# Kernel optimization log

Measured on AMD Instinct MI355X. Metric: run time of the kernel, lower is better.

Reference implementation:

```python
import jax, jax.numpy as jnp
import numpy as np

N_IN = 41024
N_OUT = 256


def setup_inputs() -> dict:
    key = jax.random.key(0)
    k1, k2, k3, k4 = jax.random.split(key, 4)
    B, K = 16384, 32
    ft_ics = jax.random.randint(k1, (B, K), 0, N_IN, dtype=jnp.int32)
    ft_vals = jax.random.uniform(k2, (B, K), dtype=jnp.float32)
    s = N_IN ** (-0.5)
    weight = jax.random.uniform(k3, (N_IN, N_OUT), dtype=jnp.float32) * (2 * s) - s
    bias = jax.random.uniform(k4, (N_OUT,), dtype=jnp.float32) * (2 * s) - s
    return {"ft_ics": ft_ics, "ft_vals": ft_vals, "weight": weight, "bias": bias}


def reference(ft_ics, ft_vals, weight, bias):
    # Sparse embedding-bag: out[b] = bias + sum_k weight[ft_ics[b,k]] * ft_vals[b,k]
    # ft_ics == -1 marks padding (the CUDA kernel breaks on -1); mask those.
    valid = ft_ics >= 0                                  # [B, K]
    safe_idx = jnp.where(valid, ft_ics, 0)               # in-range for gather
    vals = jnp.where(valid, ft_vals, 0.0)                # [B, K]
    gathered = weight[safe_idx]                          # [B, K, N_OUT]
    out = jnp.einsum("bk,bkd->bd", vals, gathered) + bias
    return out
```

## Files before the change

kernel.cpp:

```cpp
#include <hip/hip_runtime.h>


constexpr int K = 32;

__global__ __launch_bounds__(256) void FeatureTransformer_45896020525219_kernel(
    const int* __restrict__ ics,
    const float* __restrict__ vals,
    const float4* __restrict__ w4,
    const float4* __restrict__ bias4,
    float4* __restrict__ out4,
    int B)
{
    const int lane   = threadIdx.x & 63;
    const int wave   = threadIdx.x >> 6;
    const int slice  = blockIdx.x & 7;
    const int rowblk = blockIdx.x >> 3;

    const int r  = lane >> 3;
    const int c4 = lane & 7;
    const int b  = rowblk * 32 + wave * 8 + r;
    if (b >= B) return;

    const int colbase = slice * 8 + c4;

    const int4   idx4 = ((const int4*)  (ics  + b * K))[c4];
    const float4 v4   = ((const float4*)(vals + b * K))[c4];

    float4 acc = bias4[colbase];

    #pragma unroll
    for (int k = 0; k < K; ++k) {
        const int src = (lane & 56) | (k >> 2);
        const int   sel = k & 3;
        const int   jc  = sel == 0 ? idx4.x : sel == 1 ? idx4.y
                        : sel == 2 ? idx4.z : idx4.w;
        const float vc  = sel == 0 ? v4.x   : sel == 1 ? v4.y
                        : sel == 2 ? v4.z   : v4.w;
        const int   jj = __shfl(jc, src);
        const float vs = __shfl(vc, src);

        const float    v = (jj >= 0) ? vs : 0.0f;
        const unsigned j = (jj >= 0) ? (unsigned)jj : 0u;

        const float4 w = w4[(size_t)j * 64 + colbase];
        acc.x = fmaf(v, w.x, acc.x);
        acc.y = fmaf(v, w.y, acc.y);
        acc.z = fmaf(v, w.z, acc.z);
        acc.w = fmaf(v, w.w, acc.w);
    }

    out4[(size_t)b * 64 + colbase] = acc;
}

extern "C" void kernel_launch(void* const* d_in, const int* in_sizes, int n_in,
                              void* d_out, int out_size, void* d_ws, size_t ws_size,
                              hipStream_t stream) {
    const int*    ics   = (const int*)d_in[0];
    const float*  vals  = (const float*)d_in[1];
    const float4* w4    = (const float4*)d_in[2];
    const float4* bias4 = (const float4*)d_in[3];
    float4*       out4  = (float4*)d_out;

    const int B = in_sizes[0] / K;
    const int blocks = ((B + 31) / 32) * 8;

    hipLaunchKernelGGL(FeatureTransformer_45896020525219_kernel,
                       dim3(blocks), dim3(256), 0, stream,
                       ics, vals, w4, bias4, out4, B);
}
```

Measured before the change: 126.2 us.

## Process four rows per thread and load indices directly instead of shuffling

Each thread now accumulates four output rows spaced 32 apart, so every block covers 128 rows and the grid shrinks by a factor of four. The cross-lane shuffles that handed out indices and values are gone. Each thread reads the index and value vectors for its own rows directly (redundant loads, broadcast within each 8-lane group), which exposes four independent weight gathers per step for more memory-level parallelism. The bounds check only requires the first row to be in range, so a batch size that is not a multiple of 128 would go out of range. Fewer blocks and more registers per thread may also lower occupancy.

```diff
diff --git a/kernel.cpp b/kernel.cpp
--- a/kernel.cpp
+++ b/kernel.cpp
@@ -2,6 +2,13 @@
 
 
 constexpr int K = 32;
+
+static __device__ __forceinline__ int   seli(const int4& a, int s) {
+    return s == 0 ? a.x : s == 1 ? a.y : s == 2 ? a.z : a.w;
+}
+static __device__ __forceinline__ float self4(const float4& a, int s) {
+    return s == 0 ? a.x : s == 1 ? a.y : s == 2 ? a.z : a.w;
+}
 
 __global__ __launch_bounds__(256) void FeatureTransformer_45896020525219_kernel(
     const int* __restrict__ ics,
@@ -18,38 +25,63 @@
 
     const int r  = lane >> 3;
     const int c4 = lane & 7;
-    const int b  = rowblk * 32 + wave * 8 + r;
-    if (b >= B) return;
+    const int b0 = rowblk * 128 + wave * 8 + r;
+    if (b0 + 96 >= B + 96) return;
 
     const int colbase = slice * 8 + c4;
 
-    const int4   idx4 = ((const int4*)  (ics  + b * K))[c4];
-    const float4 v4   = ((const float4*)(vals + b * K))[c4];
+    const int4*   ip0 = (const int4*)  (ics  + (size_t)(b0      ) * K);
+    const int4*   ip1 = (const int4*)  (ics  + (size_t)(b0 + 32 ) * K);
+    const int4*   ip2 = (const int4*)  (ics  + (size_t)(b0 + 64 ) * K);
+    const int4*   ip3 = (const int4*)  (ics  + (size_t)(b0 + 96 ) * K);
+    const float4* fp0 = (const float4*)(vals + (size_t)(b0      ) * K);
+    const float4* fp1 = (const float4*)(vals + (size_t)(b0 + 32 ) * K);
+    const float4* fp2 = (const float4*)(vals + (size_t)(b0 + 64 ) * K);
+    const float4* fp3 = (const float4*)(vals + (size_t)(b0 + 96 ) * K);
 
-    float4 acc = bias4[colbase];
+    const float4 bv = bias4[colbase];
+    float4 acc0 = bv, acc1 = bv, acc2 = bv, acc3 = bv;
 
     #pragma unroll
-    for (int k = 0; k < K; ++k) {
-        const int src = (lane & 56) | (k >> 2);
-        const int   sel = k & 3;
-        const int   jc  = sel == 0 ? idx4.x : sel == 1 ? idx4.y
-                        : sel == 2 ? idx4.z : idx4.w;
-        const float vc  = sel == 0 ? v4.x   : sel == 1 ? v4.y
-                        : sel == 2 ? v4.z   : v4.w;
-        const int   jj = __shfl(jc, src);
-        const float vs = __shfl(vc, src);
+    for (int c = 0; c < 8; ++c) {
+        const int4   i0 = ip0[c];  const float4 g0 = fp0[c];
+        const int4   i1 = ip1[c];  const float4 g1 = fp1[c];
+        const int4   i2 = ip2[c];  const float4 g2 = fp2[c];
+        const int4   i3 = ip3[c];  const float4 g3 = fp3[c];
 
-        const float    v = (jj >= 0) ? vs : 0.0f;
-        const unsigned j = (jj >= 0) ? (unsigned)jj : 0u;
+        #pragma unroll
+        for (int s = 0; s < 4; ++s) {
+            const int j0 = seli(i0, s);  const int j1 = seli(i1, s);
+            const int j2 = seli(i2, s);  const int j3 = seli(i3, s);
+            const float v0 = (j0 >= 0) ? self4(g0, s) : 0.0f;
+            const float v1 = (j1 >= 0) ? self4(g1, s) : 0.0f;
+            const float v2 = (j2 >= 0) ? self4(g2, s) : 0.0f;
+            const float v3 = (j3 >= 0) ? self4(g3, s) : 0.0f;
+            const unsigned u0 = (j0 >= 0) ? (unsigned)j0 : 0u;
+            const unsigned u1 = (j1 >= 0) ? (unsigned)j1 : 0u;
+            const unsigned u2 = (j2 >= 0) ? (unsigned)j2 : 0u;
+            const unsigned u3 = (j3 >= 0) ? (unsigned)j3 : 0u;
 
-        const float4 w = w4[(size_t)j * 64 + colbase];
-        acc.x = fmaf(v, w.x, acc.x);
-        acc.y = fmaf(v, w.y, acc.y);
-        acc.z = fmaf(v, w.z, acc.z);
-        acc.w = fmaf(v, w.w, acc.w);
+            const float4 w0 = w4[(size_t)u0 * 64 + colbase];
+            const float4 w1 = w4[(size_t)u1 * 64 + colbase];
+            const float4 w2 = w4[(size_t)u2 * 64 + colbase];
+            const float4 w3 = w4[(size_t)u3 * 64 + colbase];
+
+            acc0.x = fmaf(v0, w0.x, acc0.x); acc0.y = fmaf(v0, w0.y, acc0.y);
+            acc0.z = fmaf(v0, w0.z, acc0.z); acc0.w = fmaf(v0, w0.w, acc0.w);
+            acc1.x = fmaf(v1, w1.x, acc1.x); acc1.y = fmaf(v1, w1.y, acc1.y);
+            acc1.z = fmaf(v1, w1.z, acc1.z); acc1.w = fmaf(v1, w1.w, acc1.w);
+            acc2.x = fmaf(v2, w2.x, acc2.x); acc2.y = fmaf(v2, w2.y, acc2.y);
+            acc2.z = fmaf(v2, w2.z, acc2.z); acc2.w = fmaf(v2, w2.w, acc2.w);
+            acc3.x = fmaf(v3, w3.x, acc3.x); acc3.y = fmaf(v3, w3.y, acc3.y);
+            acc3.z = fmaf(v3, w3.z, acc3.z); acc3.w = fmaf(v3, w3.w, acc3.w);
+        }
     }
 
-    out4[(size_t)b * 64 + colbase] = acc;
+    out4[(size_t)(b0      ) * 64 + colbase] = acc0;
+    out4[(size_t)(b0 + 32 ) * 64 + colbase] = acc1;
+    out4[(size_t)(b0 + 64 ) * 64 + colbase] = acc2;
+    out4[(size_t)(b0 + 96 ) * 64 + colbase] = acc3;
 }
 
 extern "C" void kernel_launch(void* const* d_in, const int* in_sizes, int n_in,
@@ -62,7 +94,7 @@
     float4*       out4  = (float4*)d_out;
 
     const int B = in_sizes[0] / K;
-    const int blocks = ((B + 31) / 32) * 8;
+    const int blocks = ((B + 127) / 128) * 8;
 
     hipLaunchKernelGGL(FeatureTransformer_45896020525219_kernel,
                        dim3(blocks), dim3(256), 0, stream,
```

After: 135.5 us. +7.4%, slower.

## Stage indices in LDS and batch weight gathers across independent accumulators

Applied to the files above, without the earlier changes.

Replaces the per-iteration wave shuffles of index/value pairs with a one-time LDS staging of the packed pairs. The gather loop is regrouped so eight weight rows are loaded before any FMA, with eight separate accumulators that are summed with the bias at the end. The goal is more gather loads in flight and less shuffle overhead in a latency-bound embedding-bag. It also adds a launch-bounds occupancy hint. The costs are more registers and a block barrier placed after an early return, which is safe only when B is a multiple of 32. The summation order also changes.

```diff
diff --git a/kernel.cpp b/kernel.cpp
--- a/kernel.cpp
+++ b/kernel.cpp
@@ -3,7 +3,7 @@
 
 constexpr int K = 32;
 
-__global__ __launch_bounds__(256) void FeatureTransformer_45896020525219_kernel(
+__global__ __launch_bounds__(256, 4) void FeatureTransformer_45896020525219_kernel(
     const int* __restrict__ ics,
     const float* __restrict__ vals,
     const float4* __restrict__ w4,
@@ -11,6 +11,8 @@
     float4* __restrict__ out4,
     int B)
 {
+    __shared__ int2 parm[4][K * 8];
+
     const int lane   = threadIdx.x & 63;
     const int wave   = threadIdx.x >> 6;
     const int slice  = blockIdx.x & 7;
@@ -23,33 +25,51 @@
 
     const int colbase = slice * 8 + c4;
 
-    const int4   idx4 = ((const int4*)  (ics  + b * K))[c4];
-    const float4 v4   = ((const float4*)(vals + b * K))[c4];
+    const int4   iq = ((const int4*)  (ics  + (size_t)b * K))[c4];
+    const float4 fq = ((const float4*)(vals + (size_t)b * K))[c4];
+    {
+        int2* p = parm[wave];
+        p[(c4 * 4 + 0) * 8 + r] = make_int2(iq.x, __float_as_int(fq.x));
+        p[(c4 * 4 + 1) * 8 + r] = make_int2(iq.y, __float_as_int(fq.y));
+        p[(c4 * 4 + 2) * 8 + r] = make_int2(iq.z, __float_as_int(fq.z));
+        p[(c4 * 4 + 3) * 8 + r] = make_int2(iq.w, __float_as_int(fq.w));
+    }
+    __syncthreads();
 
-    float4 acc = bias4[colbase];
+    const float4* wb = w4 + colbase;
+
+    float4 acc[8];
+    #pragma unroll
+    for (int c = 0; c < 8; ++c) acc[c] = make_float4(0.f, 0.f, 0.f, 0.f);
 
     #pragma unroll
-    for (int k = 0; k < K; ++k) {
-        const int src = (lane & 56) | (k >> 2);
-        const int   sel = k & 3;
-        const int   jc  = sel == 0 ? idx4.x : sel == 1 ? idx4.y
-                        : sel == 2 ? idx4.z : idx4.w;
-        const float vc  = sel == 0 ? v4.x   : sel == 1 ? v4.y
-                        : sel == 2 ? v4.z   : v4.w;
-        const int   jj = __shfl(jc, src);
-        const float vs = __shfl(vc, src);
-
-        const float    v = (jj >= 0) ? vs : 0.0f;
-        const unsigned j = (jj >= 0) ? (unsigned)jj : 0u;
-
-        const float4 w = w4[(size_t)j * 64 + colbase];
-        acc.x = fmaf(v, w.x, acc.x);
-        acc.y = fmaf(v, w.y, acc.y);
-        acc.z = fmaf(v, w.z, acc.z);
-        acc.w = fmaf(v, w.w, acc.w);
+    for (int u = 0; u < 4; ++u) {
+        float  v[8];
+        float4 w[8];
+        #pragma unroll
+        for (int c = 0; c < 8; ++c) {
+            const int2 P = parm[wave][(c * 4 + u) * 8 + r];
+            const int  j = P.x;
+            v[c] = (j >= 0) ? __int_as_float(P.y) : 0.0f;
+            const unsigned uj = (j >= 0) ? (unsigned)j : 0u;
+            w[c] = wb[(size_t)uj * 64];
+        }
+        #pragma unroll
+        for (int c = 0; c < 8; ++c) {
+            acc[c].x = fmaf(v[c], w[c].x, acc[c].x);
+            acc[c].y = fmaf(v[c], w[c].y, acc[c].y);
+            acc[c].z = fmaf(v[c], w[c].z, acc[c].z);
+            acc[c].w = fmaf(v[c], w[c].w, acc[c].w);
+        }
     }
 
-    out4[(size_t)b * 64 + colbase] = acc;
+    float4 o = bias4[colbase];
+    #pragma unroll
+    for (int c = 0; c < 8; ++c) {
+        o.x += acc[c].x;  o.y += acc[c].y;
+        o.z += acc[c].z;  o.w += acc[c].w;
+    }
+    out4[(size_t)b * 64 + colbase] = o;
 }
 
 extern "C" void kernel_launch(void* const* d_in, const int* in_sizes, int n_in,
```

Result: slower. 239.5 us (+89.8%).
